# Kernel optimization log

Measured on AMD Instinct MI355X. Metric: run time of the kernel, lower is better.

## Reference

```python
import jax, jax.numpy as jnp
import numpy as np

# Module hyperparameters (from init_kwargs)
START = 0.0      # lower distance cutoff
STOP = 5.0       # radius_graph cutoff r
K = 32           # max_num_neighbors
N_ATOMS = 16384
N_GRAPHS = 64
BOX = 30.0       # box edge length (Angstrom) -> realistic density for r=5 cutoff


def setup_inputs() -> dict:
    key = jax.random.key(0)
    k1, k2 = jax.random.split(key)
    pos = jax.random.uniform(k1, (N_ATOMS, 3), dtype=jnp.float32) * BOX
    batch = jnp.sort(jax.random.randint(k2, (N_ATOMS,), 0, N_GRAPHS)).astype(jnp.int64)
    return {"pos": pos, "batch": batch}


def reference(pos, batch):
    """radius_graph (loop=False) + edge vectors/norms + lower-cutoff mask.

    Because jit requires static shapes, the variable-length edge list of the
    original is returned in padded form: edge_index [2, N*K], edge_weight [N*K],
    edge_vec [N*K, 3], plus a boolean validity mask [N*K]. Valid entries match
    the original (edge_index, edge_weight, edge_vec) after compaction.
    """
    N = pos.shape[0]
    # Pairwise squared distances via the Gram trick: [N, N], memory-bound.
    sq = jnp.sum(pos * pos, axis=-1)
    d2 = sq[:, None] + sq[None, :] - 2.0 * (pos @ pos.T)
    idx = jnp.arange(N)
    valid = (batch[:, None] == batch[None, :]) \
            & (idx[:, None] != idx[None, :]) \
            & (d2 <= STOP * STOP)
    d2m = jnp.where(valid, d2, jnp.inf)
    # Up to K nearest neighbors within the radius per node.
    neg_d2, nbr = jax.lax.top_k(-d2m, K)          # [N, K]
    nbr_valid = neg_d2 > -jnp.inf                  # in-radius, same-graph, non-self
    nbr = jnp.where(nbr_valid, nbr, idx[:, None])  # pad with self (vec = 0)
    # edge_vec = pos[center] - pos[neighbor]  (pos[edge_index[0]] - pos[edge_index[1]])
    edge_vec = pos[:, None, :] - pos[nbr]          # [N, K, 3]
    sqd = jnp.sum(edge_vec * edge_vec, axis=-1)
    w = jnp.where(nbr_valid, jnp.sqrt(jnp.where(nbr_valid, sqd, 1.0)), 0.0)
    lower = nbr_valid & (w >= START)               # lower cutoff mask
    src = jnp.broadcast_to(idx[:, None], (N, K))
    edge_index = jnp.stack([src.reshape(-1), nbr.reshape(-1)])  # [2, N*K]
    mask = lower.reshape(-1)
    edge_weight = jnp.where(lower, w, 0.0).reshape(-1)
    edge_vec = jnp.where(lower[..., None], edge_vec, 0.0).reshape(-1, 3)
    return edge_index, edge_weight, edge_vec, mask
```

## Files before the change

kernel.cpp:

```cpp
#include <hip/hip_runtime.h>
#include <math.h>

#define KNBR 32
#define STOP2 25.0
#define BAND 1.0e-3f
#define CAP 64
#define WPB 4
#define APW 2
#define APB (WPB*APW)

__global__ __launch_bounds__(WPB * 64, 8)
void radius_graph_knn(const float* __restrict__ pos,
                      const int* __restrict__ batch,
                      float* __restrict__ out, int n) {
    __shared__ int jbuf[WPB][APW][CAP];
    __shared__ int win[WPB][APW][KNBR];

    const int tid  = threadIdx.x;
    const int lane = tid & 63;
    const int w    = tid >> 6;
    const int i0w  = (blockIdx.x * WPB + w) * APW;

    int ia[APW]; int ba[APW];
    float xa[APW], ya[APW], za[APW];
    #pragma unroll
    for (int a = 0; a < APW; ++a) {
        const int i = min(i0w + a, n - 1);
        ia[a] = i;
        xa[a] = pos[3 * i]; ya[a] = pos[3 * i + 1]; za[a] = pos[3 * i + 2];
        ba[a] = batch[i];
    }
    const int bFirst = ba[0];
    const int bLast  = ba[APW - 1];

    const int nchunks = (n + 63) >> 6;
    const int c0 = i0w >> 6;
    const int cw = c0 - 32 + lane;
    bool rel = false;
    if (cw >= 0 && cw < nchunks) {
        const int s = batch[cw << 6];
        const int e = batch[min(n - 1, (cw << 6) + 63)];
        rel = (s <= bLast) && (e >= bFirst);
    }
    const unsigned long long cm = __ballot(rel);
    const int cLo = c0 - 32 + (int)__builtin_ctzll(cm);
    const int cHi = c0 - 32 + (63 - (int)__builtin_clzll(cm));
    const int base = cLo << 6;
    const int stagedN = min(n, (cHi + 1) << 6) - base;

    int cnt[APW] = {0, 0};
    for (int t0 = 0; t0 < stagedN; t0 += 64) {
        const int t = t0 + lane;
        const int tc = min(t, stagedN - 1);
        const int j = base + tc;
        const float xj = pos[3 * j], yj = pos[3 * j + 1], zj = pos[3 * j + 2];
        const int bj = batch[j];
        #pragma unroll
        for (int a = 0; a < APW; ++a) {
            const float dx = xa[a] - xj, dy = ya[a] - yj, dz = za[a] - zj;
            const float d2 = dx * dx + dy * dy + dz * dz;
            const bool valid = (t < stagedN) & (j != ia[a]) & (bj == ba[a]) &
                               (d2 <= 25.0f + BAND);
            const unsigned long long m = __ballot(valid);
            const int p = cnt[a] + __popcll(m & ((1ULL << lane) - 1ULL));
            if (valid && p < CAP) jbuf[w][a][p] = j;
            cnt[a] += __popcll(m);
        }
    }

    int nsel[APW];
    #pragma unroll
    for (int a = 0; a < APW; ++a) {
        const int count = min(cnt[a], CAP);
        double d2e = 1e300;
        int jmine = 0x7fffffff;
        bool valid = false;
        if (lane < count) {
            const int j = jbuf[w][a][lane];
            const double dx = (double)xa[a] - (double)pos[3 * j];
            const double dy = (double)ya[a] - (double)pos[3 * j + 1];
            const double dz = (double)za[a] - (double)pos[3 * j + 2];
            d2e = dx * dx + dy * dy + dz * dz;
            jmine = j;
            valid = (d2e <= STOP2);
        }
        const unsigned long long vm = __ballot(valid);
        int ns = __popcll(vm);
        if (ns > KNBR) ns = KNBR;
        nsel[a] = ns;
        int rank = 0;
        for (int s = 0; s < count; ++s) {
            const double ds = __shfl(d2e, s);
            const int    js = __shfl(jmine, s);
            const bool   vs = (vm >> s) & 1ULL;
            rank += (vs && (ds < d2e || (ds == d2e && js < jmine))) ? 1 : 0;
        }
        if (valid && rank < KNBR) win[w][a][rank] = jmine;
    }

    const long long NK = (long long)n * KNBR;
    float* row0 = out;
    float* row1 = out + NK;
    float* wgt  = out + 2 * NK;
    float* vec  = out + 3 * NK;
    float* msk  = out + 6 * NK;

    const int a = lane >> 5;
    const int s = lane & 31;
    const int   i  = a ? ia[1] : ia[0];
    const float xi = a ? xa[1] : xa[0];
    const float yi = a ? ya[1] : ya[0];
    const float zi = a ? za[1] : za[0];
    const int   ns = a ? nsel[1] : nsel[0];
    const bool v = s < ns;
    const int j = v ? win[w][a][s] : i;
    const float vx = xi - pos[3 * j];
    const float vy = yi - pos[3 * j + 1];
    const float vz = zi - pos[3 * j + 2];
    const float ww = v ? sqrtf(vx * vx + vy * vy + vz * vz) : 0.0f;
    const long long o = (long long)i * KNBR + s;
    row0[o] = (float)i;
    row1[o] = (float)j;
    wgt[o]  = ww;
    vec[3 * o + 0] = v ? vx : 0.0f;
    vec[3 * o + 1] = v ? vy : 0.0f;
    vec[3 * o + 2] = v ? vz : 0.0f;
    msk[o]  = v ? 1.0f : 0.0f;
}

extern "C" void kernel_launch(void* const* d_in, const int* in_sizes, int n_in,
                              void* d_out, int out_size, void* d_ws, size_t ws_size,
                              hipStream_t stream) {
    const float* pos   = (const float*)d_in[0];
    const int*   batch = (const int*)d_in[1];
    float* out = (float*)d_out;
    int n = in_sizes[1];

    const int block = WPB * 64;
    const int grid = (n + APB - 1) / APB;
    radius_graph_knn<<<grid, block, 0, stream>>>(pos, batch, out, n);
}
```

Before: 69.17 us.

## Prefetch next candidate chunk and rank both atoms concurrently in half-waves

The candidate scan now software-prefetches the next chunk's positions and batch ids while the current chunk is tested, aiming to hide global load latency. When both atoms have at most 32 candidates, the ranking step processes the two atoms at once, one per 32-lane half-wave, using width-32 shuffles. This halves the serial shuffle loops in the common case. A fallback keeps the old per-atom path for larger candidate counts, at the cost of more code and registers.

Result: no change. 68.73 us (-0.6%).

```diff
diff --git a/kernel.cpp b/kernel.cpp
--- a/kernel.cpp
+++ b/kernel.cpp
@@ -21,17 +21,10 @@
     const int w    = tid >> 6;
     const int i0w  = (blockIdx.x * WPB + w) * APW;
 
-    int ia[APW]; int ba[APW];
-    float xa[APW], ya[APW], za[APW];
-    #pragma unroll
-    for (int a = 0; a < APW; ++a) {
-        const int i = min(i0w + a, n - 1);
-        ia[a] = i;
-        xa[a] = pos[3 * i]; ya[a] = pos[3 * i + 1]; za[a] = pos[3 * i + 2];
-        ba[a] = batch[i];
-    }
-    const int bFirst = ba[0];
-    const int bLast  = ba[APW - 1];
+    const int i0 = min(i0w, n - 1), i1 = min(i0w + 1, n - 1);
+    const float x0 = pos[3 * i0], y0 = pos[3 * i0 + 1], z0 = pos[3 * i0 + 2];
+    const float x1 = pos[3 * i1], y1 = pos[3 * i1 + 1], z1 = pos[3 * i1 + 2];
+    const int b0 = batch[i0], b1 = batch[i1];
 
     const int nchunks = (n + 63) >> 6;
     const int c0 = i0w >> 6;
@@ -40,7 +33,7 @@
     if (cw >= 0 && cw < nchunks) {
         const int s = batch[cw << 6];
         const int e = batch[min(n - 1, (cw << 6) + 63)];
-        rel = (s <= bLast) && (e >= bFirst);
+        rel = (s <= b1) && (e >= b0);
     }
     const unsigned long long cm = __ballot(rel);
     const int cLo = c0 - 32 + (int)__builtin_ctzll(cm);
@@ -48,54 +41,115 @@
     const int base = cLo << 6;
     const int stagedN = min(n, (cHi + 1) << 6) - base;
 
-    int cnt[APW] = {0, 0};
+    int cnt0 = 0, cnt1 = 0;
+    float xj, yj, zj; int bj;
+    {
+        const int tc = min(lane, stagedN - 1);
+        const int j = base + tc;
+        xj = pos[3 * j]; yj = pos[3 * j + 1]; zj = pos[3 * j + 2];
+        bj = batch[j];
+    }
     for (int t0 = 0; t0 < stagedN; t0 += 64) {
+        float xn = 0.f, yn = 0.f, zn = 0.f; int bn = 0;
+        const int t0n = t0 + 64;
+        if (t0n < stagedN) {
+            const int tcn = min(t0n + lane, stagedN - 1);
+            const int jn = base + tcn;
+            xn = pos[3 * jn]; yn = pos[3 * jn + 1]; zn = pos[3 * jn + 2];
+            bn = batch[jn];
+        }
         const int t = t0 + lane;
-        const int tc = min(t, stagedN - 1);
-        const int j = base + tc;
-        const float xj = pos[3 * j], yj = pos[3 * j + 1], zj = pos[3 * j + 2];
-        const int bj = batch[j];
-        #pragma unroll
-        for (int a = 0; a < APW; ++a) {
-            const float dx = xa[a] - xj, dy = ya[a] - yj, dz = za[a] - zj;
+        const int j = base + min(t, stagedN - 1);
+        {
+            const float dx = x0 - xj, dy = y0 - yj, dz = z0 - zj;
             const float d2 = dx * dx + dy * dy + dz * dz;
-            const bool valid = (t < stagedN) & (j != ia[a]) & (bj == ba[a]) &
+            const bool valid = (t < stagedN) & (j != i0) & (bj == b0) &
                                (d2 <= 25.0f + BAND);
             const unsigned long long m = __ballot(valid);
-            const int p = cnt[a] + __popcll(m & ((1ULL << lane) - 1ULL));
-            if (valid && p < CAP) jbuf[w][a][p] = j;
-            cnt[a] += __popcll(m);
+            const int p = cnt0 + __popcll(m & ((1ULL << lane) - 1ULL));
+            if (valid && p < CAP) jbuf[w][0][p] = j;
+            cnt0 += __popcll(m);
         }
+        {
+            const float dx = x1 - xj, dy = y1 - yj, dz = z1 - zj;
+            const float d2 = dx * dx + dy * dy + dz * dz;
+            const bool valid = (t < stagedN) & (j != i1) & (bj == b1) &
+                               (d2 <= 25.0f + BAND);
+            const unsigned long long m = __ballot(valid);
+            const int p = cnt1 + __popcll(m & ((1ULL << lane) - 1ULL));
+            if (valid && p < CAP) jbuf[w][1][p] = j;
+            cnt1 += __popcll(m);
+        }
+        xj = xn; yj = yn; zj = zn; bj = bn;
     }
 
-    int nsel[APW];
-    #pragma unroll
-    for (int a = 0; a < APW; ++a) {
-        const int count = min(cnt[a], CAP);
+    const int count0 = min(cnt0, CAP);
+    const int count1 = min(cnt1, CAP);
+    const int a = lane >> 5;
+    const int q = lane & 31;
+    const float xi = a ? x1 : x0, yi = a ? y1 : y0, zi = a ? z1 : z0;
+    const int   ii = a ? i1 : i0;
+    int ns_my = 0;
+
+    if (count0 <= 32 && count1 <= 32) {
+        const int cmy = a ? count1 : count0;
         double d2e = 1e300;
         int jmine = 0x7fffffff;
         bool valid = false;
-        if (lane < count) {
-            const int j = jbuf[w][a][lane];
-            const double dx = (double)xa[a] - (double)pos[3 * j];
-            const double dy = (double)ya[a] - (double)pos[3 * j + 1];
-            const double dz = (double)za[a] - (double)pos[3 * j + 2];
+        if (q < cmy) {
+            const int j = jbuf[w][a][q];
+            const double dx = (double)xi - (double)pos[3 * j];
+            const double dy = (double)yi - (double)pos[3 * j + 1];
+            const double dz = (double)zi - (double)pos[3 * j + 2];
             d2e = dx * dx + dy * dy + dz * dz;
             jmine = j;
             valid = (d2e <= STOP2);
         }
         const unsigned long long vm = __ballot(valid);
-        int ns = __popcll(vm);
-        if (ns > KNBR) ns = KNBR;
-        nsel[a] = ns;
+        const unsigned int vmh = (unsigned int)(vm >> (a ? 32 : 0));
+        ns_my = __popc(vmh);
+        const int cmax = max(count0, count1);
         int rank = 0;
-        for (int s = 0; s < count; ++s) {
-            const double ds = __shfl(d2e, s);
-            const int    js = __shfl(jmine, s);
-            const bool   vs = (vm >> s) & 1ULL;
+        for (int s = 0; s < cmax; ++s) {
+            const double ds = __shfl(d2e, s, 32);
+            const int    js = __shfl(jmine, s, 32);
+            const bool   vs = (vmh >> s) & 1u;
             rank += (vs && (ds < d2e || (ds == d2e && js < jmine))) ? 1 : 0;
         }
         if (valid && rank < KNBR) win[w][a][rank] = jmine;
+    } else {
+        int nsel0 = 0, nsel1 = 0;
+        for (int aa = 0; aa < APW; ++aa) {
+            const int count = aa ? count1 : count0;
+            const float xA = aa ? x1 : x0, yA = aa ? y1 : y0, zA = aa ? z1 : z0;
+            const int   iA = aa ? i1 : i0;
+            double d2e = 1e300;
+            int jmine = 0x7fffffff;
+            bool valid = false;
+            if (lane < count) {
+                const int j = jbuf[w][aa][lane];
+                const double dx = (double)xA - (double)pos[3 * j];
+                const double dy = (double)yA - (double)pos[3 * j + 1];
+                const double dz = (double)zA - (double)pos[3 * j + 2];
+                d2e = dx * dx + dy * dy + dz * dz;
+                jmine = j;
+                valid = (d2e <= STOP2);
+            }
+            (void)iA;
+            const unsigned long long vm = __ballot(valid);
+            int ns = __popcll(vm);
+            if (ns > KNBR) ns = KNBR;
+            if (aa) nsel1 = ns; else nsel0 = ns;
+            int rank = 0;
+            for (int s = 0; s < count; ++s) {
+                const double ds = __shfl(d2e, s);
+                const int    js = __shfl(jmine, s);
+                const bool   vs = (vm >> s) & 1ULL;
+                rank += (vs && (ds < d2e || (ds == d2e && js < jmine))) ? 1 : 0;
+            }
+            if (valid && rank < KNBR) win[w][aa][rank] = jmine;
+        }
+        ns_my = a ? nsel1 : nsel0;
     }
 
     const long long NK = (long long)n * KNBR;
@@ -105,21 +159,14 @@
     float* vec  = out + 3 * NK;
     float* msk  = out + 6 * NK;
 
-    const int a = lane >> 5;
-    const int s = lane & 31;
-    const int   i  = a ? ia[1] : ia[0];
-    const float xi = a ? xa[1] : xa[0];
-    const float yi = a ? ya[1] : ya[0];
-    const float zi = a ? za[1] : za[0];
-    const int   ns = a ? nsel[1] : nsel[0];
-    const bool v = s < ns;
-    const int j = v ? win[w][a][s] : i;
+    const bool v = q < ns_my;
+    const int j = v ? win[w][a][q] : ii;
     const float vx = xi - pos[3 * j];
     const float vy = yi - pos[3 * j + 1];
     const float vz = zi - pos[3 * j + 2];
     const float ww = v ? sqrtf(vx * vx + vy * vy + vz * vz) : 0.0f;
-    const long long o = (long long)i * KNBR + s;
-    row0[o] = (float)i;
+    const long long o = (long long)ii * KNBR + q;
+    row0[o] = (float)ii;
     row1[o] = (float)j;
     wgt[o]  = ww;
     vec[3 * o + 0] = v ? vx : 0.0f;
```
